# Kernel optimization log

Measured on AMD Instinct MI355X. Metric: run time of the kernel, lower is better.

The kernel has to match this reference:

```python
import jax, jax.numpy as jnp
import numpy as np

B, CTX, DRAFT, D = 2, 4096, 512, 2048
H, KVH, HD = 16, 4, 128
N_REP = H // KVH
EPS = 1e-6
THETA = 10000.0
SCALE = 1.0 / np.sqrt(HD).astype(np.float32)


def setup_inputs() -> dict:
    key = jax.random.key(0)
    ks = jax.random.split(key, 6)
    return {
        "draft_hidden": jax.random.normal(ks[0], (B, DRAFT, D), jnp.float32),
        "context_hidden": jax.random.normal(ks[1], (B, CTX, D), jnp.float32),
        "Wq": jax.random.normal(ks[2], (H * HD, D), jnp.float32) * 0.02,
        "Wk": jax.random.normal(ks[3], (KVH * HD, D), jnp.float32) * 0.02,
        "Wv": jax.random.normal(ks[4], (KVH * HD, D), jnp.float32) * 0.02,
        "Wo": jax.random.normal(ks[5], (D, H * HD), jnp.float32) * 0.02,
        "q_norm_w": jnp.ones((HD,), jnp.float32),
        "k_norm_w": jnp.ones((HD,), jnp.float32),
        "context_position_ids": jnp.broadcast_to(jnp.arange(CTX, dtype=jnp.int32), (B, CTX)),
        "draft_position_ids": jnp.broadcast_to(CTX + jnp.arange(DRAFT, dtype=jnp.int32), (B, DRAFT)),
    }


def _rms_norm(x, w):
    # per-head RMSNorm over last dim (head_dim), computed in fp32
    v = jnp.mean(jnp.square(x.astype(jnp.float32)), axis=-1, keepdims=True)
    return (w * (x.astype(jnp.float32) * jax.lax.rsqrt(v + EPS))).astype(x.dtype)


def _rotate_half(x):
    x1, x2 = jnp.split(x, 2, axis=-1)
    return jnp.concatenate((-x2, x1), axis=-1)


def _rope(x, pos):
    # x: [B, nH, S, HD], pos: [B, S] int -> cos/sin gathered per position
    inv_freq = 1.0 / (THETA ** (jnp.arange(0, HD, 2, dtype=jnp.float32) / HD))  # [HD/2]
    freqs = pos.astype(jnp.float32)[:, None, :, None] * inv_freq  # [B,1,S,HD/2]
    emb = jnp.concatenate((freqs, freqs), axis=-1)  # [B,1,S,HD]
    return x * jnp.cos(emb) + _rotate_half(x) * jnp.sin(emb)


def reference(draft_hidden, context_hidden, Wq, Wk, Wv, Wo, q_norm_w, k_norm_w,
              context_position_ids, draft_position_ids):
    bsz, draft_len, _ = draft_hidden.shape
    ctx_len = context_hidden.shape[1]
    total_len = ctx_len + draft_len

    # Q from draft hidden only
    q = (draft_hidden @ Wq.T).reshape(bsz, draft_len, H, HD)
    q = _rms_norm(q, q_norm_w).transpose(0, 2, 1, 3)  # [B,H,Sq,HD]

    # Dual-source KV: context then draft, shared projections
    kv_in = jnp.concatenate([context_hidden, draft_hidden], axis=1)  # [B,total,D]
    k = (kv_in @ Wk.T).reshape(bsz, total_len, KVH, HD)
    v = (kv_in @ Wv.T).reshape(bsz, total_len, KVH, HD).transpose(0, 2, 1, 3)
    k = _rms_norm(k, k_norm_w).transpose(0, 2, 1, 3)  # [B,KVH,total,HD]

    full_position_ids = jnp.concatenate([context_position_ids, draft_position_ids], axis=1)
    q = _rope(q, draft_position_ids)
    k = _rope(k, full_position_ids)

    # GQA expansion (repeat each kv head n_rep times contiguously)
    k = jnp.repeat(k, N_REP, axis=1)  # [B,H,total,HD]
    v = jnp.repeat(v, N_REP, axis=1)

    # full (unmasked) scaled dot-product attention, block_mask=None path
    scores = jnp.einsum('bhqd,bhkd->bhqk', q, k) * SCALE
    probs = jax.nn.softmax(scores, axis=-1)
    attn = jnp.einsum('bhqk,bhkd->bhqd', probs, v)  # [B,H,Sq,HD]

    attn = attn.transpose(0, 2, 1, 3).reshape(bsz, draft_len, H * HD)
    return attn @ Wo.T
```

## Files before the change

kernel.cpp:

```cpp
#include <hip/hip_runtime.h>
#include <stdint.h>

#define B_ 2
#define CTX_ 4096
#define DRAFT_ 512
#define D_ 2048
#define H_ 16
#define KVH_ 4
#define HD_ 128
#define TOT_ 4608
#define NSPLIT 4
#define SPLIT_LEN (TOT_ / NSPLIT)

using bf16x8 = __attribute__((ext_vector_type(8))) short;
using f32x4  = __attribute__((ext_vector_type(4))) float;
using f32x16 = __attribute__((ext_vector_type(16))) float;

__device__ __forceinline__ unsigned short f2bf(float x) {
  unsigned int u = __float_as_uint(x);
  u += 0x7fffu + ((u >> 16) & 1u);
  return (unsigned short)(u >> 16);
}

__device__ __forceinline__ unsigned cvtpk(float lo, float hi) {
  unsigned r;
  asm("v_cvt_pk_bf16_f32 %0, %1, %2" : "=v"(r) : "v"(lo), "v"(hi));
  return r;
}

__device__ __forceinline__ void gload16(const void* g, void* l) {
  __builtin_amdgcn_global_load_lds((const __attribute__((address_space(1))) void*)g,
                                   (__attribute__((address_space(3))) void*)l, 16, 0, 0);
}

__device__ __forceinline__ f32x16 vbroad16(float x) {
  f32x16 v;
#pragma unroll
  for (int i = 0; i < 16; ++i) v[i] = x;
  return v;
}

__global__ __launch_bounds__(256, 4)
void conv_kernel(const float* __restrict__ ctx, const float* __restrict__ draft,
                 const float* __restrict__ wq, const float* __restrict__ wk,
                 const float* __restrict__ wv, const float* __restrict__ wo,
                 unsigned short* __restrict__ kv, unsigned short* __restrict__ wqb,
                 unsigned short* __restrict__ wkb, unsigned short* __restrict__ wvb,
                 unsigned short* __restrict__ wob) {
  long t = (long)blockIdx.x * 256 + threadIdx.x;
  const long NKV = (long)B_ * TOT_ * D_ / 8;
  const long NWQ = 2048L * 2048 / 8;
  const long NWK = 512L * 2048 / 8;
  const float* src;
  unsigned short* dst;
  if (t < NKV) {
    long i = t * 8;
    int b = (int)(i / ((long)TOT_ * D_));
    long rem = i - (long)b * TOT_ * D_;
    int r = (int)(rem / D_);
    int c = (int)(rem - (long)r * D_);
    if (r < CTX_) src = ctx + ((long)(b * CTX_ + r)) * D_ + c;
    else          src = draft + ((long)(b * DRAFT_ + (r - CTX_))) * D_ + c;
    dst = kv + i;
  } else if (t < NKV + NWQ) {
    long l = t - NKV; src = wq + l * 8; dst = wqb + l * 8;
  } else if (t < NKV + NWQ + NWK) {
    long l = t - NKV - NWQ; src = wk + l * 8; dst = wkb + l * 8;
  } else if (t < NKV + NWQ + 2 * NWK) {
    long l = t - NKV - NWQ - NWK; src = wv + l * 8; dst = wvb + l * 8;
  } else {
    long l = t - NKV - NWQ - 2 * NWK; src = wo + l * 8; dst = wob + l * 8;
  }
  float4 a = ((const float4*)src)[0];
  float4 b4 = ((const float4*)src)[1];
  uint4 o;
  o.x = (unsigned)f2bf(a.x) | ((unsigned)f2bf(a.y) << 16);
  o.y = (unsigned)f2bf(a.z) | ((unsigned)f2bf(a.w) << 16);
  o.z = (unsigned)f2bf(b4.x) | ((unsigned)f2bf(b4.y) << 16);
  o.w = (unsigned)f2bf(b4.z) | ((unsigned)f2bf(b4.w) << 16);
  *((uint4*)dst) = o;
}

template <int BM, int BN, bool TO_LDS = false>
__device__ __forceinline__ void gemm_body(const unsigned short* __restrict__ A,
                                          const unsigned short* __restrict__ W,
                                          float* __restrict__ C, int ld, int kLen,
                                          int N, unsigned short* lds) {
  constexpr int MT = BM / 32;
  constexpr int NT = BN / 32;
  constexpr int BUF = (BM + BN) * 64;
  constexpr int LOADS = BM / 32 + BN / 32;
  const int tid = threadIdx.x;
  const int lane = tid & 63, wid = tid >> 6;
  const int g = lane >> 4, r16 = lane & 15;
  const int wm = wid >> 1, wn = wid & 1;

  f32x4 zero = {0.f, 0.f, 0.f, 0.f};
  f32x4 acc[MT][NT];
#pragma unroll
  for (int i = 0; i < MT; ++i)
#pragma unroll
    for (int j = 0; j < NT; ++j) acc[i][j] = zero;

  auto stage = [&](int kb, unsigned short* buf) {
    unsigned short* As = buf;
    unsigned short* Bs = buf + BM * 64;
#pragma unroll
    for (int is = 0; is < BM / 32; ++is) {
      int row = is * 32 + (tid >> 3);
      int sl = (tid & 7) ^ (row & 7);
      gload16(A + (long)row * ld + kb + sl * 8, As + is * 2048 + wid * 512);
    }
#pragma unroll
    for (int is = 0; is < BN / 32; ++is) {
      int row = is * 32 + (tid >> 3);
      int sl = (tid & 7) ^ (row & 7);
      gload16(W + (long)row * ld + kb + sl * 8, Bs + is * 2048 + wid * 512);
    }
  };

  stage(0, lds);
  const int nk = kLen >> 6;
  for (int t = 0; t < nk; ++t) {
    if (t + 1 < nk) {
      stage((t + 1) << 6, lds + ((t + 1) & 1) * BUF);
      if constexpr (LOADS == 8)      asm volatile("s_waitcnt vmcnt(8)" ::: "memory");
      else if constexpr (LOADS == 6) asm volatile("s_waitcnt vmcnt(6)" ::: "memory");
      else if constexpr (LOADS == 4) asm volatile("s_waitcnt vmcnt(4)" ::: "memory");
      else                           asm volatile("s_waitcnt vmcnt(0)" ::: "memory");
    } else {
      asm volatile("s_waitcnt vmcnt(0)" ::: "memory");
    }
    __builtin_amdgcn_s_barrier();
    __builtin_amdgcn_sched_barrier(0);
    unsigned short* As = lds + (t & 1) * BUF;
    unsigned short* Bs = As + BM * 64;
#pragma unroll
    for (int kh = 0; kh < 2; ++kh) {
      bf16x8 af[MT], bfr[NT];
#pragma unroll
      for (int i = 0; i < MT; ++i) {
        int row = wm * (BM / 2) + i * 16 + r16;
        int sl = (kh * 4 + g) ^ (row & 7);
        af[i] = *(const bf16x8*)(As + row * 64 + sl * 8);
      }
#pragma unroll
      for (int j = 0; j < NT; ++j) {
        int row = wn * (BN / 2) + j * 16 + r16;
        int sl = (kh * 4 + g) ^ (row & 7);
        bfr[j] = *(const bf16x8*)(Bs + row * 64 + sl * 8);
      }
#pragma unroll
      for (int i = 0; i < MT; ++i)
#pragma unroll
        for (int j = 0; j < NT; ++j)
          acc[i][j] = __builtin_amdgcn_mfma_f32_16x16x32_bf16(af[i], bfr[j], acc[i][j], 0, 0, 0);
    }
    __builtin_amdgcn_sched_barrier(0);
    __builtin_amdgcn_s_barrier();
  }
  if constexpr (TO_LDS) {
    float* F = (float*)lds;
#pragma unroll
    for (int i = 0; i < MT; ++i)
#pragma unroll
      for (int j = 0; j < NT; ++j)
#pragma unroll
        for (int e = 0; e < 4; ++e)
          F[(wm * 64 + i * 16 + g * 4 + e) * 128 + wn * 64 + j * 16 + r16] = acc[i][j][e];
  } else {
#pragma unroll
    for (int i = 0; i < MT; ++i)
#pragma unroll
      for (int j = 0; j < NT; ++j)
#pragma unroll
        for (int e = 0; e < 4; ++e) {
          int row = wm * (BM / 2) + i * 16 + g * 4 + e;
          int col = wn * (BN / 2) + j * 16 + r16;
          C[(long)row * N + col] = acc[i][j][e];
        }
  }
}

__global__ __launch_bounds__(256, 2)
void qkv_kernel(const unsigned short* __restrict__ kvb,
                const unsigned short* __restrict__ wqb,
                const unsigned short* __restrict__ wkvb, float* __restrict__ qraw,
                float* __restrict__ kvraw, unsigned short* __restrict__ vt) {
  __shared__ unsigned short lds[2 * 256 * 64];
  const int tid = threadIdx.x;
  int id = (blockIdx.x & 7) * 88 + (blockIdx.x >> 3);
  if (id < 128) {
    int b = id >> 6, mb = (id >> 4) & 3, nb = id & 15;
    const unsigned short* A = kvb + ((long)b * TOT_ + CTX_ + mb * 128) * 2048;
    const unsigned short* W = wqb + (long)nb * 128 * 2048;
    float* C = qraw + ((long)b * 512 + mb * 128) * 2048 + nb * 128;
    gemm_body<128, 128>(A, W, C, 2048, 2048, 2048, lds);
  } else {
    int id2 = id - 128;
    int mb = id2 >> 3, nb = id2 & 7;
    const unsigned short* A = kvb + (long)mb * 128 * 2048;
    const unsigned short* W = wkvb + (long)nb * 128 * 2048;
    if (nb < 4) {
      float* C = kvraw + (long)mb * 128 * 1024 + nb * 128;
      gemm_body<128, 128>(A, W, C, 2048, 2048, 1024, lds);
    } else {
      gemm_body<128, 128, true>(A, W, nullptr, 2048, 2048, 0, lds);
      __syncthreads();
      float* F = (float*)lds;
      int bb = mb / 36;
      int sbase = (mb % 36) * 128;
      int kvh = nb - 4;
      int d = tid & 127;
      int g0 = tid >> 7;
      unsigned short* vrow = vt + ((long)((bb * KVH_ + kvh) * 128 + d)) * TOT_;
#pragma unroll
      for (int gi = 0; gi < 8; ++gi) {
        int s0 = (g0 + 2 * gi) * 8;
        unsigned o[4];
#pragma unroll
        for (int jj = 0; jj < 4; ++jj) {
          unsigned short lo = f2bf(F[(s0 + 2 * jj) * 128 + d]);
          unsigned short hi = f2bf(F[(s0 + 2 * jj + 1) * 128 + d]);
          o[jj] = (unsigned)lo | ((unsigned)hi << 16);
        }
        int k0 = s0 & 63;
        long dstbase = sbase + (s0 & ~63) + (k0 & 48) + ((k0 & 8) >> 1);
        *(uint2*)(vrow + dstbase) = make_uint2(o[0], o[1]);
        *(uint2*)(vrow + dstbase + 8) = make_uint2(o[2], o[3]);
      }
    }
  }
}

__global__ __launch_bounds__(256, 3)
void ogemm_kernel(const unsigned short* __restrict__ attb,
                  const unsigned short* __restrict__ wob, float* __restrict__ out) {
  __shared__ unsigned short lds[2 * 128 * 64];
  int sw = (blockIdx.x & 7) * 64 + (blockIdx.x >> 3);
  int nb = sw >> 4, mb = sw & 15;
  const unsigned short* A = attb + (long)mb * 64 * 2048;
  const unsigned short* W = wob + (long)nb * 64 * 2048;
  float* C = out + (long)mb * 64 * 2048 + nb * 64;
  gemm_body<64, 64>(A, W, C, 2048, 2048, 2048, lds);
}

__global__ __launch_bounds__(256, 4)
void post_kernel(const float* __restrict__ qraw, const float* __restrict__ kvraw,
                 const float* __restrict__ qw, const float* __restrict__ kw,
                 const int* __restrict__ cpos, const int* __restrict__ dpos,
                 unsigned short* __restrict__ qatt, unsigned short* __restrict__ katt) {
  const int QB = (B_ * DRAFT_ * H_) / 4;
  int bid = blockIdx.x;
  int tid = threadIdx.x;
  int lane = tid & 63, wid = tid >> 6;
  bool isQ = (bid < QB);
  int row = (isQ ? bid : bid - QB) * 4 + wid;
  const float* src;
  const float* wnorm;
  int pos;
  float fold;
  unsigned short* dst;
  if (isQ) {
    int b = row >> 13;
    int r2 = row & 8191;
    int s = r2 >> 4, hh = r2 & 15;
    src = qraw + (long)row * 128;
    wnorm = qw;
    pos = dpos[b * DRAFT_ + s];
    fold = 0.08838834764831843f * 1.4426950408889634f;
    dst = qatt + ((long)(b * H_ + hh) * DRAFT_ + s) * 128;
  } else {
    int b = row / (TOT_ * KVH_);
    int r2 = row - b * (TOT_ * KVH_);
    int s = r2 >> 2, hh = r2 & 3;
    src = kvraw + ((long)(b * TOT_ + s)) * 1024 + hh * 128;
    wnorm = kw;
    pos = (s < CTX_) ? cpos[b * CTX_ + s] : dpos[b * DRAFT_ + (s - CTX_)];
    fold = 1.0f;
    dst = katt + ((long)(b * KVH_ + hh) * TOT_ + s) * 128;
  }
  float x1 = src[lane], x2 = src[lane + 64];
  float ss = x1 * x1 + x2 * x2;
#pragma unroll
  for (int off = 1; off < 64; off <<= 1) ss += __shfl_xor(ss, off);
  float rn = rsqrtf(ss * 0.0078125f + 1e-6f);
  float y1 = wnorm[lane] * x1 * rn;
  float y2 = wnorm[lane + 64] * x2 * rn;
  float invf = exp2f((float)lane * -0.20762050593046014f);
  float fr = (float)pos * invf;
  float sn, cs;
  sincosf(fr, &sn, &cs);
  dst[lane] = f2bf((y1 * cs - y2 * sn) * fold);
  dst[lane + 64] = f2bf((y2 * cs + y1 * sn) * fold);
}

__global__ __launch_bounds__(512, 2)
void attn_kernel(const unsigned short* __restrict__ Q, const unsigned short* __restrict__ Kt,
                 const unsigned short* __restrict__ Vt, float* __restrict__ pO,
                 float* __restrict__ pL) {
  __shared__ unsigned short lds[2 * 16384];
  const int tid = threadIdx.x, lane = tid & 63, wid = tid >> 6;
  const int hi = lane >> 5, l31 = lane & 31;
  int sw = ((blockIdx.x & 7) << 5) | (blockIdx.x >> 3);
  const int q0 = sw & 1, h = (sw >> 1) & 15, z = sw >> 5;
  const int b = z >> 2, split = z & 3;
  const int kvh = h >> 2;
  const float M = 16.4f;

  const unsigned short* Qb =
      Q + ((long)(b * H_ + h) * DRAFT_ + q0 * 256 + wid * 32) * 128;
  bf16x8 qf[8];
#pragma unroll
  for (int ks = 0; ks < 8; ++ks)
    qf[ks] = *(const bf16x8*)(Qb + l31 * 128 + ks * 16 + hi * 8);

  f32x16 acc[4];
#pragma unroll
  for (int nb = 0; nb < 4; ++nb) acc[nb] = vbroad16(0.f);
  float l_run = 0.0f;

  const unsigned short* Kbase = Kt + (long)(b * KVH_ + kvh) * TOT_ * 128;
  const unsigned short* Vbase = Vt + (long)(b * KVH_ + kvh) * 128L * TOT_;

  auto stage = [&](int s0, int c) {
    unsigned short* Ks = lds + c * 16384;
    unsigned short* Vs = Ks + 8192;
#pragma unroll
    for (int is = 0; is < 2; ++is) {
      int row = is * 32 + (tid >> 4);
      int sl = (tid & 15) ^ (row & 7);
      gload16(Kbase + (long)(s0 + row) * 128 + sl * 8, Ks + is * 4096 + wid * 512);
    }
#pragma unroll
    for (int is = 0; is < 2; ++is) {
      int d = is * 64 + (tid >> 3);
      int sl = (tid & 7) ^ (d & 7);
      gload16(Vbase + (long)d * TOT_ + s0 + sl * 8, Vs + is * 4096 + wid * 512);
    }
  };

  const int sBeg = split * SPLIT_LEN;
  const int NTile = SPLIT_LEN / 64;
  stage(sBeg, 0);
  int cur = 0;
  for (int t = 0; t < NTile; ++t) {
    if (t + 1 < NTile) {
      stage(sBeg + (t + 1) * 64, cur ^ 1);
      asm volatile("s_waitcnt vmcnt(4)" ::: "memory");
    } else {
      asm volatile("s_waitcnt vmcnt(0)" ::: "memory");
    }
    __builtin_amdgcn_s_barrier();
    __builtin_amdgcn_sched_barrier(0);
    const char* KsB = (const char*)(lds + cur * 16384);
    const char* VsB = KsB + 16384;

    f32x16 st0 = vbroad16(-M), st1 = vbroad16(-M);
    __builtin_amdgcn_s_setprio(1);
#pragma unroll
    for (int ks = 0; ks < 8; ++ks) {
      int gsl = ks * 2 + hi;
      bf16x8 a0 = *(const bf16x8*)(KsB + l31 * 256 + ((gsl ^ (l31 & 7)) * 16));
      bf16x8 a1 = *(const bf16x8*)(KsB + (32 + l31) * 256 + ((gsl ^ (l31 & 7)) * 16));
      st0 = __builtin_amdgcn_mfma_f32_32x32x16_bf16(a0, qf[ks], st0, 0, 0, 0);
      st1 = __builtin_amdgcn_mfma_f32_32x32x16_bf16(a1, qf[ks], st1, 0, 0, 0);
    }
    __builtin_amdgcn_s_setprio(0);

    float l_own = 0.0f;
    unsigned pkA[8];
#pragma unroll
    for (int m = 0; m < 8; ++m) {
      float e0 = exp2f(st0[2 * m]), e1 = exp2f(st0[2 * m + 1]);
      l_own += e0 + e1;
      pkA[m] = cvtpk(e0, e1);
    }
    union { unsigned u[4]; bf16x8 v; } pf01[2], pf23[2];
#pragma unroll
    for (int m = 0; m < 4; ++m) {
      pf01[0].u[m] = pkA[m];
      pf01[1].u[m] = pkA[m + 4];
    }
    __builtin_amdgcn_s_setprio(1);
#pragma unroll
    for (int nb = 0; nb < 4; ++nb) {
      int d = nb * 32 + l31;
#pragma unroll
      for (int k2 = 0; k2 < 2; ++k2) {
        bf16x8 a = *(const bf16x8*)(VsB + d * 128 + (((k2 * 2 + hi) ^ (d & 7)) * 16));
        acc[nb] = __builtin_amdgcn_mfma_f32_32x32x16_bf16(a, pf01[k2].v, acc[nb], 0, 0, 0);
      }
    }
    __builtin_amdgcn_sched_barrier(0);
    unsigned pkB[8];
#pragma unroll
    for (int m = 0; m < 8; ++m) {
      float e0 = exp2f(st1[2 * m]), e1 = exp2f(st1[2 * m + 1]);
      l_own += e0 + e1;
      pkB[m] = cvtpk(e0, e1);
    }
#pragma unroll
    for (int m = 0; m < 4; ++m) {
      pf23[0].u[m] = pkB[m];
      pf23[1].u[m] = pkB[m + 4];
    }
    l_run += l_own;
#pragma unroll
    for (int nb = 0; nb < 4; ++nb) {
      int d = nb * 32 + l31;
#pragma unroll
      for (int k2 = 0; k2 < 2; ++k2) {
        bf16x8 a = *(const bf16x8*)(VsB + d * 128 + ((((k2 + 2) * 2 + hi) ^ (d & 7)) * 16));
        acc[nb] = __builtin_amdgcn_mfma_f32_32x32x16_bf16(a, pf23[k2].v, acc[nb], 0, 0, 0);
      }
    }
    __builtin_amdgcn_s_setprio(0);
    __builtin_amdgcn_sched_barrier(0);
    __builtin_amdgcn_s_barrier();
    cur ^= 1;
  }
  l_run += __shfl_xor(l_run, 32);

  const long R = (long)B_ * H_ * DRAFT_;
  const int q = q0 * 256 + wid * 32 + l31;
  const long rowIdx = ((long)(b * H_ + h)) * DRAFT_ + q;
  const long pbase = ((long)split * R + rowIdx) * 128;
#pragma unroll
  for (int nb = 0; nb < 4; ++nb)
#pragma unroll
    for (int r4 = 0; r4 < 4; ++r4) {
      int d0 = nb * 32 + 8 * r4 + 4 * hi;
      float4 v = make_float4(acc[nb][4 * r4 + 0], acc[nb][4 * r4 + 1],
                             acc[nb][4 * r4 + 2], acc[nb][4 * r4 + 3]);
      *(float4*)(pO + pbase + d0) = v;
    }
  if (hi == 0) pL[(long)split * R + rowIdx] = l_run;
}

__global__ __launch_bounds__(256, 4)
void acomb_kernel(const float* __restrict__ pO, const float* __restrict__ pL,
                  unsigned short* __restrict__ attb) {
  const long R = (long)B_ * H_ * DRAFT_;
  int row = blockIdx.x * 2 + (threadIdx.x >> 7);
  int d = threadIdx.x & 127;
  float ltot = 0.0f, o = 0.0f;
#pragma unroll
  for (int i = 0; i < NSPLIT; ++i) {
    ltot += pL[(long)i * R + row];
    o += pO[((long)i * R + row) * 128 + d];
  }
  o /= ltot;
  int bh = row >> 9, q = row & 511;
  int b = bh >> 4, h = bh & 15;
  attb[(((long)(b * 512 + q) * 16 + h)) * 128 + d] = f2bf(o);
}

extern "C" void kernel_launch(void* const* d_in, const int* in_sizes, int n_in,
                              void* d_out, int out_size, void* d_ws, size_t ws_size,
                              hipStream_t stream) {
  const float* draft = (const float*)d_in[0];
  const float* ctx = (const float*)d_in[1];
  const float* Wq = (const float*)d_in[2];
  const float* Wk = (const float*)d_in[3];
  const float* Wv = (const float*)d_in[4];
  const float* Wo = (const float*)d_in[5];
  const float* qw = (const float*)d_in[6];
  const float* kw = (const float*)d_in[7];
  const int* cpos = (const int*)d_in[8];
  const int* dpos = (const int*)d_in[9];

  char* ws = (char*)d_ws;
  unsigned short* kvb = (unsigned short*)(ws + 0);
  unsigned short* wqb = (unsigned short*)(ws + 37748736);
  unsigned short* wkb = (unsigned short*)(ws + 46137344);
  unsigned short* wvb = (unsigned short*)(ws + 48234496);
  unsigned short* wob = (unsigned short*)(ws + 50331648);
  float* qraw = (float*)(ws + 58720256);
  float* kvraw = (float*)(ws + 67108864);
  float* pO = (float*)(ws + 67108864);
  float* pL = (float*)(ws + 100663296);
  unsigned short* qatt = (unsigned short*)(ws + 104857600);
  unsigned short* katt = (unsigned short*)(ws + 109051904);
  unsigned short* vtb = (unsigned short*)(ws + 118489088);
  unsigned short* attb = (unsigned short*)(ws + 127926272);

  conv_kernel<<<dim3(14336), 256, 0, stream>>>(ctx, draft, Wq, Wk, Wv, Wo, kvb, wqb,
                                               wkb, wvb, wob);
  qkv_kernel<<<dim3(704), 256, 0, stream>>>(kvb, wqb, wkb, qraw, kvraw, vtb);
  post_kernel<<<dim3(13312), 256, 0, stream>>>(qraw, kvraw, qw, kw, cpos, dpos, qatt,
                                               katt);
  attn_kernel<<<dim3(256), 512, 0, stream>>>(qatt, katt, vtb, pO, pL);
  acomb_kernel<<<dim3(8192), 256, 0, stream>>>(pO, pL, attb);
  ogemm_kernel<<<dim3(512), 256, 0, stream>>>(attb, wob, (float*)d_out);
}
```

Baseline: 171.4 us.

## Shrink QKV GEMM LDS footprint with single-buffered B to raise occupancy

After: 167.7 us. 1.02x faster.

```diff
diff --git a/kernel.cpp b/kernel.cpp
--- a/kernel.cpp
+++ b/kernel.cpp
@@ -81,7 +81,7 @@
   *((uint4*)dst) = o;
 }
 
-template <int BM, int BN, bool TO_LDS = false>
+template <int BM, int BN>
 __device__ __forceinline__ void gemm_body(const unsigned short* __restrict__ A,
                                           const unsigned short* __restrict__ W,
                                           float* __restrict__ C, int ld, int kLen,
@@ -159,35 +159,119 @@
     __builtin_amdgcn_sched_barrier(0);
     __builtin_amdgcn_s_barrier();
   }
+#pragma unroll
+  for (int i = 0; i < MT; ++i)
+#pragma unroll
+    for (int j = 0; j < NT; ++j)
+#pragma unroll
+      for (int e = 0; e < 4; ++e) {
+        int row = wm * (BM / 2) + i * 16 + g * 4 + e;
+        int col = wn * (BN / 2) + j * 16 + r16;
+        C[(long)row * N + col] = acc[i][j][e];
+      }
+}
+
+template <bool TO_LDS>
+__device__ __forceinline__ void gemm_qkv(const unsigned short* __restrict__ A,
+                                         const unsigned short* __restrict__ W,
+                                         float* __restrict__ C, int N,
+                                         unsigned short* lds) {
+  const int tid = threadIdx.x;
+  const int lane = tid & 63, wid = tid >> 6;
+  const int g = lane >> 4, r16 = lane & 15;
+  const int wm = wid >> 1, wn = wid & 1;
+
+  f32x4 zero = {0.f, 0.f, 0.f, 0.f};
+  f32x4 acc[4][4];
+#pragma unroll
+  for (int i = 0; i < 4; ++i)
+#pragma unroll
+    for (int j = 0; j < 4; ++j) acc[i][j] = zero;
+
+  auto stageA = [&](int kb, int c) {
+#pragma unroll
+    for (int is = 0; is < 4; ++is) {
+      int row = is * 32 + (tid >> 3);
+      int sl = (tid & 7) ^ (row & 7);
+      gload16(A + (long)row * 2048 + kb + sl * 8, lds + c * 8192 + is * 2048 + wid * 512);
+    }
+  };
+  auto stageB = [&](int kb) {
+#pragma unroll
+    for (int is = 0; is < 4; ++is) {
+      int row = is * 32 + (tid >> 3);
+      int sl = (tid & 7) ^ (row & 7);
+      gload16(W + (long)row * 2048 + kb + sl * 8, lds + 16384 + is * 2048 + wid * 512);
+    }
+  };
+
+  stageA(0, 0);
+  for (int t = 0; t < 32; ++t) {
+    stageB(t << 6);
+    if (t + 1 < 32) {
+      stageA((t + 1) << 6, (t + 1) & 1);
+      asm volatile("s_waitcnt vmcnt(4)" ::: "memory");
+    } else {
+      asm volatile("s_waitcnt vmcnt(0)" ::: "memory");
+    }
+    __builtin_amdgcn_s_barrier();
+    __builtin_amdgcn_sched_barrier(0);
+    const unsigned short* As = lds + (t & 1) * 8192;
+    const unsigned short* Bs = lds + 16384;
+#pragma unroll
+    for (int kh = 0; kh < 2; ++kh) {
+      bf16x8 af[4], bfr[4];
+#pragma unroll
+      for (int i = 0; i < 4; ++i) {
+        int row = wm * 64 + i * 16 + r16;
+        int sl = (kh * 4 + g) ^ (row & 7);
+        af[i] = *(const bf16x8*)(As + row * 64 + sl * 8);
+      }
+#pragma unroll
+      for (int j = 0; j < 4; ++j) {
+        int row = wn * 64 + j * 16 + r16;
+        int sl = (kh * 4 + g) ^ (row & 7);
+        bfr[j] = *(const bf16x8*)(Bs + row * 64 + sl * 8);
+      }
+#pragma unroll
+      for (int i = 0; i < 4; ++i)
+#pragma unroll
+        for (int j = 0; j < 4; ++j)
+          acc[i][j] = __builtin_amdgcn_mfma_f32_16x16x32_bf16(af[i], bfr[j], acc[i][j], 0, 0, 0);
+    }
+    __builtin_amdgcn_sched_barrier(0);
+    __builtin_amdgcn_s_barrier();
+  }
   if constexpr (TO_LDS) {
-    float* F = (float*)lds;
-#pragma unroll
-    for (int i = 0; i < MT; ++i)
-#pragma unroll
-      for (int j = 0; j < NT; ++j)
+    unsigned short* Fb = lds;
+#pragma unroll
+    for (int i = 0; i < 4; ++i)
+#pragma unroll
+      for (int j = 0; j < 4; ++j)
 #pragma unroll
         for (int e = 0; e < 4; ++e)
-          F[(wm * 64 + i * 16 + g * 4 + e) * 128 + wn * 64 + j * 16 + r16] = acc[i][j][e];
+          Fb[(wm * 64 + i * 16 + g * 4 + e) * 128 + wn * 64 + j * 16 + r16] =
+              f2bf(acc[i][j][e]);
   } else {
 #pragma unroll
-    for (int i = 0; i < MT; ++i)
-#pragma unroll
-      for (int j = 0; j < NT; ++j)
+    for (int i = 0; i < 4; ++i)
+#pragma unroll
+      for (int j = 0; j < 4; ++j)
 #pragma unroll
         for (int e = 0; e < 4; ++e) {
-          int row = wm * (BM / 2) + i * 16 + g * 4 + e;
-          int col = wn * (BN / 2) + j * 16 + r16;
+          int row = wm * 64 + i * 16 + g * 4 + e;
+          int col = wn * 64 + j * 16 + r16;
           C[(long)row * N + col] = acc[i][j][e];
         }
   }
 }
 
-__global__ __launch_bounds__(256, 2)
+__global__ __launch_bounds__(256, 3)
 void qkv_kernel(const unsigned short* __restrict__ kvb,
                 const unsigned short* __restrict__ wqb,
                 const unsigned short* __restrict__ wkvb, float* __restrict__ qraw,
                 float* __restrict__ kvraw, unsigned short* __restrict__ vt) {
-  __shared__ unsigned short lds[2 * 256 * 64];
+  __shared__ unsigned short lds[24576];
   const int tid = threadIdx.x;
   int id = (blockIdx.x & 7) * 88 + (blockIdx.x >> 3);
   if (id < 128) {
@@ -195,7 +279,7 @@
     const unsigned short* A = kvb + ((long)b * TOT_ + CTX_ + mb * 128) * 2048;
     const unsigned short* W = wqb + (long)nb * 128 * 2048;
     float* C = qraw + ((long)b * 512 + mb * 128) * 2048 + nb * 128;
-    gemm_body<128, 128>(A, W, C, 2048, 2048, 2048, lds);
+    gemm_qkv<false>(A, W, C, 2048, lds);
   } else {
     int id2 = id - 128;
     int mb = id2 >> 3, nb = id2 & 7;
@@ -203,11 +287,11 @@
     const unsigned short* W = wkvb + (long)nb * 128 * 2048;
     if (nb < 4) {
       float* C = kvraw + (long)mb * 128 * 1024 + nb * 128;
-      gemm_body<128, 128>(A, W, C, 2048, 2048, 1024, lds);
+      gemm_qkv<false>(A, W, C, 1024, lds);
     } else {
-      gemm_body<128, 128, true>(A, W, nullptr, 2048, 2048, 0, lds);
+      gemm_qkv<true>(A, W, nullptr, 0, lds);
       __syncthreads();
-      float* F = (float*)lds;
+      const unsigned short* Fb = lds;
       int bb = mb / 36;
       int sbase = (mb % 36) * 128;
       int kvh = nb - 4;
@@ -220,8 +304,8 @@
         unsigned o[4];
 #pragma unroll
         for (int jj = 0; jj < 4; ++jj) {
-          unsigned short lo = f2bf(F[(s0 + 2 * jj) * 128 + d]);
-          unsigned short hi = f2bf(F[(s0 + 2 * jj + 1) * 128 + d]);
+          unsigned short lo = Fb[(s0 + 2 * jj) * 128 + d];
+          unsigned short hi = Fb[(s0 + 2 * jj + 1) * 128 + d];
           o[jj] = (unsigned)lo | ((unsigned)hi << 16);
         }
         int k0 = s0 & 63;
```
